# Performance work log

Hardware: AMD Instinct MI355X
Metric: run time of the kernel (lower is better)

Reference implementation:

```python
import jax, jax.numpy as jnp
import numpy as np

EMBED_DIM = 1024
N_HEAD = 16
HEAD_DIM = EMBED_DIM // N_HEAD
B, S = 2, 2048


def setup_inputs() -> dict:
    key = jax.random.key(0)
    ks = jax.random.split(key, 11)
    d = EMBED_DIM
    scale = 1.0 / np.sqrt(d)
    inp = {
        "query_inp": jax.random.normal(ks[0], (B, S, d), dtype=jnp.float32),
        "key_inp": jax.random.normal(ks[1], (B, S, d), dtype=jnp.float32),
        "value_inp": jax.random.normal(ks[2], (B, S, d), dtype=jnp.float32),
        "Wq": jax.random.normal(ks[3], (d, d), dtype=jnp.float32) * scale,
        "bq": jnp.zeros((d,), dtype=jnp.float32),
        "Wk": jax.random.normal(ks[4], (d, d), dtype=jnp.float32) * scale,
        "bk": jnp.zeros((d,), dtype=jnp.float32),
        "Wv": jax.random.normal(ks[5], (d, d), dtype=jnp.float32) * scale,
        "bv": jnp.zeros((d,), dtype=jnp.float32),
        "Wo": jax.random.normal(ks[6], (d, d), dtype=jnp.float32) * scale,
        "bo": jnp.zeros((d,), dtype=jnp.float32),
    }
    return inp


def reference(query_inp, key_inp, value_inp, Wq, bq, Wk, bk, Wv, bv, Wo, bo):
    b, s, _ = query_inp.shape
    # Linear projections (weights stored as [in, out]); split heads -> [b, h, s, hd]
    def proj(x, W, bias):
        y = jnp.einsum("bsd,de->bse", x, W) + bias
        return y.reshape(b, s, N_HEAD, HEAD_DIM).transpose(0, 2, 1, 3)

    q = proj(query_inp, Wq, bq)
    k = proj(key_inp, Wk, bk)
    v = proj(value_inp, Wv, bv)

    scores = jnp.einsum("bhqd,bhkd->bhqk", q, k) / jnp.sqrt(
        jnp.asarray(HEAD_DIM, dtype=q.dtype)
    )
    attn = jax.nn.softmax(scores, axis=-1)
    out = jnp.einsum("bhqk,bhkd->bhqd", attn, v)  # [b, h, s, hd]
    out = out.transpose(0, 2, 1, 3).reshape(b, s, EMBED_DIM)
    return jnp.einsum("bsd,de->bse", out, Wo) + bo
```

## Files before the change

### kernel.cpp

```cpp
#include <hip/hip_runtime.h>


typedef __bf16 bf16;
typedef __bf16 bf16x4 __attribute__((ext_vector_type(4)));
typedef __bf16 bf16x8 __attribute__((ext_vector_type(8)));
typedef float f32x4 __attribute__((ext_vector_type(4)));

#define DEV static __device__ __forceinline__

constexpr int D = 1024;
constexpr int NH = 16;
constexpr int HD = 64;
constexpr int B_ = 2;
constexpr int S_ = 2048;
constexpr size_t MAT = (size_t)D * D;
constexpr size_t XSZ = (size_t)B_ * S_ * D;

DEV void glds16(const bf16* g, bf16* l) {
  __builtin_amdgcn_global_load_lds(
      (__attribute__((address_space(1))) void*)g,
      (__attribute__((address_space(3))) void*)l, 16, 0, 0);
}

DEV int detect_isf(const unsigned short* wq16, int tid) {
  const unsigned short v = wq16[tid & 63];
  const bool hot = ((v >> 7) & 0xFF) >= 0x90;
  return (__ballot(hot) != 0ull) ? 1 : 0;
}

__global__ __launch_bounds__(256) void prep_kernel(
    const void* __restrict__ X0, const void* __restrict__ X1, const void* __restrict__ X2,
    const void* __restrict__ W0, const void* __restrict__ W1,
    const void* __restrict__ W2, const void* __restrict__ W3,
    const void* __restrict__ b0, const void* __restrict__ b1,
    const void* __restrict__ b2, const void* __restrict__ b3,
    const unsigned short* __restrict__ wq16,
    bf16* __restrict__ Xc, bf16* __restrict__ WT4, bf16* __restrict__ bc) {
  __shared__ bf16 t[64][65];
  const int tid = threadIdx.x;
  const int isf = detect_isf(wq16, tid);
  const int blk = blockIdx.x;

  if (blk < 12288) {
    const int mat = blk >> 12;
    const int bx = blk & 4095;
    const void* s = (mat == 0) ? X0 : (mat == 1) ? X1 : X2;
    const size_t vi = (size_t)bx * 256 + tid;
    bf16* dst = Xc + (size_t)mat * XSZ + vi * 4;
    if (isf) {
      const float4 f = ((const float4*)s)[vi];
      bf16x4 o = {(bf16)f.x, (bf16)f.y, (bf16)f.z, (bf16)f.w};
      *(bf16x4*)dst = o;
    } else {
      *(bf16x4*)dst = *(const bf16x4*)((const bf16*)s + vi * 4);
    }
  } else if (blk < 13312) {
    const int idx = blk - 12288;
    const int mat = idx >> 8;
    const int rem = idx & 255;
    const void* W = (mat == 0) ? W0 : (mat == 1) ? W1 : (mat == 2) ? W2 : W3;
    bf16* o = WT4 + (size_t)mat * MAT;
    const int r0 = (rem >> 4) * 64, c0 = (rem & 15) * 64;
#pragma unroll
    for (int e = 0; e < 16; e++) {
      const int ii = tid + e * 256;
      const size_t gi = (size_t)(r0 + (ii >> 6)) * D + c0 + (ii & 63);
      t[ii >> 6][ii & 63] = isf ? (bf16)((const float*)W)[gi] : ((const bf16*)W)[gi];
    }
    __syncthreads();
#pragma unroll
    for (int e = 0; e < 16; e++) {
      const int ii = tid + e * 256;
      const int co = ii >> 6, ro = ii & 63;
      o[(size_t)(c0 + co) * D + r0 + ro] = t[ro][co];
    }
  } else {
    const int mat = blk - 13312;
    const void* s = (mat == 0) ? b0 : (mat == 1) ? b1 : (mat == 2) ? b2 : b3;
    bf16* dst = bc + mat * 1024;
    for (int i = tid; i < 1024; i += 256)
      dst[i] = isf ? (bf16)((const float*)s)[i] : ((const bf16*)s)[i];
  }
}

DEV void gemm_core(const bf16* __restrict__ A, const bf16* __restrict__ WT,
                   int m0, int n0, bf16* As, bf16* Bs, f32x4 acc[4][4]) {
  const int tid = threadIdx.x;
  const int w = tid >> 6, lane = tid & 63;
  const int ln = lane & 15, qd = lane >> 4;
  const int wr = w >> 1, wc = w & 1;
  const int l8r = lane >> 3, l8c = lane & 7;
  const int swz8 = ((l8c ^ l8r) * 8);

#pragma unroll
  for (int i = 0; i < 4; i++)
#pragma unroll
    for (int j = 0; j < 4; j++) acc[i][j] = (f32x4){0.f, 0.f, 0.f, 0.f};

  for (int k0 = 0; k0 < D; k0 += 64) {
    __syncthreads();
#pragma unroll
    for (int t = 0; t < 4; t++) {
      const int c = w * 4 + t;
      glds16(A + (size_t)(m0 + c * 8 + l8r) * D + k0 + swz8, As + c * 512);
      glds16(WT + (size_t)(n0 + c * 8 + l8r) * D + k0 + swz8, Bs + c * 512);
    }
    __syncthreads();
#pragma unroll
    for (int ks = 0; ks < 2; ks++) {
      bf16x8 af[4], bfr[4];
#pragma unroll
      for (int i = 0; i < 4; i++)
        af[i] = *(const bf16x8*)(As + (wr * 64 + i * 16 + ln) * 64 +
                                 (((ks * 4 + qd) ^ (ln & 7)) * 8));
#pragma unroll
      for (int j = 0; j < 4; j++)
        bfr[j] = *(const bf16x8*)(Bs + (wc * 64 + j * 16 + ln) * 64 +
                                  (((ks * 4 + qd) ^ (ln & 7)) * 8));
#pragma unroll
      for (int i = 0; i < 4; i++)
#pragma unroll
        for (int j = 0; j < 4; j++)
          acc[i][j] = __builtin_amdgcn_mfma_f32_16x16x32_bf16(af[i], bfr[j], acc[i][j], 0, 0, 0);
    }
  }
}

__global__ __launch_bounds__(256) void qkv_kernel(
    const bf16* __restrict__ Xc, const bf16* __restrict__ WT4, const bf16* __restrict__ bc,
    bf16* __restrict__ Qb, bf16* __restrict__ Kb, bf16* __restrict__ Vb) {
  __shared__ __align__(16) bf16 SMEM[128 * 128];
  bf16* As = SMEM;
  bf16* Bs = SMEM + 8192;
  const int mt = blockIdx.x;
  const int nb = blockIdx.y;
  const int mat = nb >> 3;
  const int n0 = (nb & 7) * 128;
  const bf16* A = Xc + (size_t)mat * XSZ;
  const bf16* WT = WT4 + (size_t)mat * MAT;
  const bf16* bias = bc + mat * 1024;

  f32x4 acc[4][4];
  gemm_core(A, WT, mt * 128, n0, As, Bs, acc);

  const int tid = threadIdx.x;
  const int w = tid >> 6, lane = tid & 63;
  const int ln = lane & 15, qd = lane >> 4;
  const int wr = w >> 1, wc = w & 1;
  bf16* dst = (mat == 0) ? Qb : (mat == 1) ? Kb : Vb;
  const float scale = (mat == 0) ? 0.180336880f : 1.0f;

  if (mat == 2) {
#pragma unroll
    for (int i = 0; i < 4; i++)
#pragma unroll
      for (int j = 0; j < 4; j++) {
        const int col = n0 + wc * 64 + j * 16 + ln;
        const float bb = (float)bias[col];
        const int h = col >> 6, dd = col & 63;
        const int tok0 = mt * 128 + wr * 64 + i * 16 + qd * 4;
        const int b = tok0 >> 11, s0 = tok0 & (S_ - 1);
        bf16* base = dst + (size_t)(b * NH + h) * S_ * HD;
        bf16x4 pv;
#pragma unroll
        for (int r = 0; r < 4; r++) pv[r] = (bf16)(acc[i][j][r] + bb);
        const size_t off = ((size_t)((dd >> 4) * (S_ >> 5) + (s0 >> 5))) * 512 +
                           ((s0 >> 3) & 3) * 128 + (dd & 15) * 8 + (s0 & 7);
        *(bf16x4*)(base + off) = pv;
      }
  } else {
    __syncthreads();
#pragma unroll
    for (int i = 0; i < 4; i++)
#pragma unroll
      for (int j = 0; j < 4; j++) {
        const int col_local = wc * 64 + j * 16 + ln;
        const float bb = (float)bias[n0 + col_local];
        const int cdd = col_local >> 3, c7 = col_local & 7;
#pragma unroll
        for (int r = 0; r < 4; r++) {
          const int s_local = wr * 64 + i * 16 + qd * 4 + r;
          SMEM[s_local * 128 + ((cdd ^ (s_local & 15)) * 8) + c7] =
              (bf16)((acc[i][j][r] + bb) * scale);
        }
      }
    __syncthreads();
    const int run = tid >> 1;
    const int row16 = run >> 4;
    const int c = run & 15;
    const int hh = (n0 >> 6) + (c >> 3);
    const int b = mt >> 4;
    bf16* gbase = dst + (size_t)(b * NH + hh) * S_ * HD +
                  (size_t)((mt & 15) * 8 + row16) * 1024 + (c & 7) * 128;
    const int sh = (tid & 1) * 8;
#pragma unroll
    for (int e = 0; e < 8; e++) {
      const int srem = sh + e;
      const bf16x8 v =
          *(const bf16x8*)(SMEM + (row16 * 16 + srem) * 128 + ((c ^ srem) & 15) * 8);
      *(bf16x8*)(gbase + srem * 8) = v;
    }
  }
}

__global__ __launch_bounds__(256, 3) void attn_kernel(const bf16* __restrict__ Qb,
                                                      const bf16* __restrict__ Kb,
                                                      const bf16* __restrict__ Vb,
                                                      bf16* __restrict__ Opart,
                                                      float* __restrict__ lbuf) {
  __shared__ __align__(16) bf16 KVs[2][8192];
  __shared__ __align__(16) bf16 P2[64 * 128];

  const int bh = blockIdx.x;
  const int qt = blockIdx.y;
  const int sp = blockIdx.z;
  const int tid = threadIdx.x;
  const int w = tid >> 6, lane = tid & 63;
  const int ln = lane & 15, qd = lane >> 4;

  const size_t base = (size_t)bh * S_ * HD;
  const int q0 = qt * 64;
  const bf16* Kp = Kb + base;
  const bf16* Vp = Vb + base;
  const bf16* Qp = Qb + base;
  bf16* Pw = P2 + (w * 16) * 128;

  bf16x8 qf[2];
#pragma unroll
  for (int t = 0; t < 2; t++)
    qf[t] = *(const bf16x8*)(Qp + (size_t)(qt * 4 + w) * 1024 + (t * 4 + qd) * 128 + ln * 8);

  f32x4 acc_o[4];
#pragma unroll
  for (int j = 0; j < 4; j++) acc_o[j] = (f32x4){0.f, 0.f, 0.f, 0.f};
  float l_i = 0.f;

  const int kbeg = sp * (S_ / 2), kend = kbeg + (S_ / 2);

#define STAGE_KV(buf, k0)                                                              \
  {                                                                                    \
    bf16* Ks_ = &KVs[buf][0];                                                          \
    bf16* Vs_ = &KVs[buf][4096];                                                       \
    _Pragma("unroll") for (int e = 0; e < 2; e++) {                                    \
      const int seg = w * 2 + e;                                                       \
      glds16(Kp + (size_t)((k0) >> 4) * 1024 + seg * 512 + lane * 8, Ks_ + seg * 512); \
    }                                                                                  \
    _Pragma("unroll") for (int s = 0; s < 2; s++) {                                    \
      glds16(Vp + (size_t)(w * (S_ >> 5) + ((k0) >> 5) + s) * 512 + lane * 8,          \
             Vs_ + (w * 2 + s) * 512);                                                 \
    }                                                                                  \
  }

  STAGE_KV(0, kbeg);
  __syncthreads();

  int cur = 0;
  for (int k0 = kbeg; k0 < kend; k0 += 64) {
    if (k0 + 64 < kend) STAGE_KV(cur ^ 1, k0 + 64);

    const bf16* Ks = &KVs[cur][0];
    const bf16* Vs = &KVs[cur][4096];

    f32x4 st[4];
#pragma unroll
    for (int j = 0; j < 4; j++) st[j] = (f32x4){0.f, 0.f, 0.f, 0.f};

    {
      bf16x8 kf[8];
#pragma unroll
      for (int t = 0; t < 2; t++)
#pragma unroll
        for (int j = 0; j < 4; j++)
          kf[t * 4 + j] = *(const bf16x8*)(Ks + j * 1024 + (t * 4 + qd) * 128 + ln * 8);
      __builtin_amdgcn_s_setprio(1);
#pragma unroll
      for (int t = 0; t < 2; t++)
#pragma unroll
        for (int j = 0; j < 4; j++)
          st[j] = __builtin_amdgcn_mfma_f32_16x16x32_bf16(kf[t * 4 + j], qf[t], st[j], 0, 0, 0);
      __builtin_amdgcn_s_setprio(0);
    }

    {
      float rs = 0.f;
#pragma unroll
      for (int j = 0; j < 4; j++)
#pragma unroll
        for (int r = 0; r < 4; r++) {
          const float p = __builtin_amdgcn_exp2f(st[j][r]);
          st[j][r] = p;
          rs += p;
        }
      rs += __shfl_xor(rs, 16);
      rs += __shfl_xor(rs, 32);
      l_i += rs;

      bf16* pr = Pw + ln * 128;
#pragma unroll
      for (int j = 0; j < 4; j++) {
        bf16x4 pv;
#pragma unroll
        for (int r = 0; r < 4; r++) pv[r] = (bf16)st[j][r];
        const int c0 = j * 2 + (qd >> 1);
        *(bf16x4*)(pr + (((c0 + ln) & 15) * 8) + (qd & 1) * 4) = pv;
      }
    }

#pragma unroll
    for (int s = 0; s < 2; s++) {
      bf16x8 vf[4];
#pragma unroll
      for (int jn = 0; jn < 4; jn++)
        vf[jn] = *(const bf16x8*)(Vs + (jn * 2 + s) * 512 + qd * 128 + ln * 8);
      const bf16x8 pf =
          *(const bf16x8*)(Pw + ln * 128 + (((s * 4 + qd + ln) & 15) * 8));
      __builtin_amdgcn_s_setprio(1);
#pragma unroll
      for (int jn = 0; jn < 4; jn++)
        acc_o[jn] = __builtin_amdgcn_mfma_f32_16x16x32_bf16(pf, vf[jn], acc_o[jn], 0, 0, 0);
      __builtin_amdgcn_s_setprio(0);
    }

    __syncthreads();
    cur ^= 1;
  }

  bf16* tw = Pw;
#pragma unroll
  for (int jn = 0; jn < 4; jn++)
#pragma unroll
    for (int r = 0; r < 4; r++)
      tw[(qd * 4 + r) * 72 + jn * 16 + ln] = (bf16)acc_o[jn][r];
  bf16* Og = Opart + (size_t)sp * XSZ + base + (size_t)(q0 + w * 16) * HD;
#pragma unroll
  for (int p = 0; p < 2; p++) {
    const int ql = p * 8 + (lane >> 3);
    const int seg = lane & 7;
    const bf16x8 vv = *(const bf16x8*)(tw + ql * 72 + seg * 8);
    *(bf16x8*)(Og + (size_t)ql * 64 + seg * 8) = vv;
  }
  if (qd == 0)
    lbuf[((size_t)sp * 32 + bh) * S_ + q0 + w * 16 + ln] = l_i;
#undef STAGE_KV
}

__global__ __launch_bounds__(256) void merge_k(const bf16* __restrict__ Opart,
                                               const float* __restrict__ lbuf,
                                               bf16* __restrict__ Ob) {
  const int gid = blockIdx.x * 256 + threadIdx.x;
  const int seg = gid & 7;
  const int row = gid >> 3;
  const int bh = row >> 11, q = row & 2047;
  const float l0 = lbuf[row];
  const float l1 = lbuf[32 * S_ + row];
  const float inv = 1.0f / (l0 + l1);
  const bf16x8 a = *(const bf16x8*)(Opart + (size_t)row * 64 + seg * 8);
  const bf16x8 c = *(const bf16x8*)(Opart + XSZ + (size_t)row * 64 + seg * 8);
  bf16x8 o;
#pragma unroll
  for (int r = 0; r < 8; r++) o[r] = (bf16)(((float)a[r] + (float)c[r]) * inv);
  const int b = bh >> 4, h = bh & 15;
  *(bf16x8*)(Ob + ((size_t)(b * S_ + q)) * D + h * HD + seg * 8) = o;
}

__global__ __launch_bounds__(256) void oproj_kernel(const bf16* __restrict__ Ob,
                                                    const bf16* __restrict__ WoT,
                                                    const bf16* __restrict__ bo,
                                                    const unsigned short* __restrict__ wq16,
                                                    void* __restrict__ outv) {
  __shared__ __align__(16) bf16 As[128 * 64];
  __shared__ __align__(16) bf16 Bs[128 * 64];
  const int isf = detect_isf(wq16, threadIdx.x);
  const int mt = blockIdx.x, nb = blockIdx.y;
  f32x4 acc[4][4];
  gemm_core(Ob, WoT, mt * 128, nb * 128, As, Bs, acc);
  const int tid = threadIdx.x;
  const int w = tid >> 6, lane = tid & 63;
  const int ln = lane & 15, qd = lane >> 4;
  const int wr = w >> 1, wc = w & 1;
#pragma unroll
  for (int i = 0; i < 4; i++)
#pragma unroll
    for (int j = 0; j < 4; j++) {
      const int col = nb * 128 + wc * 64 + j * 16 + ln;
      const float bb = (float)bo[col];
#pragma unroll
      for (int r = 0; r < 4; r++) {
        const int tok = mt * 128 + wr * 64 + i * 16 + qd * 4 + r;
        const float v = acc[i][j][r] + bb;
        const size_t oi = (size_t)tok * D + col;
        if (isf) ((float*)outv)[oi] = v;
        else ((bf16*)outv)[oi] = (bf16)v;
      }
    }
}

extern "C" void kernel_launch(void* const* d_in, const int* in_sizes, int n_in,
                              void* d_out, int out_size, void* d_ws, size_t ws_size,
                              hipStream_t stream) {
  bf16* ws = (bf16*)d_ws;

  bf16* WT4 = ws;
  bf16* Xc  = WT4 + 4 * MAT;
  bf16* bc  = Xc + 3 * XSZ;
  bf16* Qb  = bc + 4096;
  bf16* Kb  = Qb + XSZ;
  bf16* Vb  = Kb + XSZ;
  bf16* Ob  = Vb + XSZ;
  bf16*  Opart = Xc;
  float* lbuf  = (float*)(Xc + 2 * XSZ);

  const unsigned short* wq16 = (const unsigned short*)d_in[3];

  prep_kernel<<<13316, 256, 0, stream>>>(d_in[0], d_in[1], d_in[2],
                                         d_in[3], d_in[5], d_in[7], d_in[9],
                                         d_in[4], d_in[6], d_in[8], d_in[10],
                                         wq16, Xc, WT4, bc);
  qkv_kernel<<<dim3(32, 24), 256, 0, stream>>>(Xc, WT4, bc, Qb, Kb, Vb);
  attn_kernel<<<dim3(32, 32, 2), 256, 0, stream>>>(Qb, Kb, Vb, Opart, lbuf);
  merge_k<<<2048, 256, 0, stream>>>(Opart, lbuf, Ob);
  oproj_kernel<<<dim3(32, 8), 256, 0, stream>>>(Ob, WT4 + 3 * MAT, bc + 3 * 1024, wq16, d_out);
}
```

Measured before the change: 253.4 us.

## Drop split-K attention and merge kernel; normalize output inside attention

Attention blocks now walk the full key length instead of splitting it in two. Each block normalizes its own output by the row sum and writes straight into the head-interleaved Ob layout. This removes the partial-output and row-sum writes, the separate merge kernel launch and its global memory round trip. In exchange the grid halves to 1024 blocks, which lowers parallelism and lengthens each block's serial loop over keys.

```diff
diff --git a/kernel.cpp b/kernel.cpp
--- a/kernel.cpp
+++ b/kernel.cpp
@@ -206,14 +206,12 @@
 __global__ __launch_bounds__(256, 3) void attn_kernel(const bf16* __restrict__ Qb,
                                                       const bf16* __restrict__ Kb,
                                                       const bf16* __restrict__ Vb,
-                                                      bf16* __restrict__ Opart,
-                                                      float* __restrict__ lbuf) {
+                                                      bf16* __restrict__ Ob) {
   __shared__ __align__(16) bf16 KVs[2][8192];
   __shared__ __align__(16) bf16 P2[64 * 128];
 
   const int bh = blockIdx.x;
   const int qt = blockIdx.y;
-  const int sp = blockIdx.z;
   const int tid = threadIdx.x;
   const int w = tid >> 6, lane = tid & 63;
   const int ln = lane & 15, qd = lane >> 4;
@@ -234,8 +232,6 @@
 #pragma unroll
   for (int j = 0; j < 4; j++) acc_o[j] = (f32x4){0.f, 0.f, 0.f, 0.f};
   float l_i = 0.f;
-
-  const int kbeg = sp * (S_ / 2), kend = kbeg + (S_ / 2);
 
 #define STAGE_KV(buf, k0)                                                              \
   {                                                                                    \
@@ -251,12 +247,12 @@
     }                                                                                  \
   }
 
-  STAGE_KV(0, kbeg);
+  STAGE_KV(0, 0);
   __syncthreads();
 
   int cur = 0;
-  for (int k0 = kbeg; k0 < kend; k0 += 64) {
-    if (k0 + 64 < kend) STAGE_KV(cur ^ 1, k0 + 64);
+  for (int k0 = 0; k0 < S_; k0 += 64) {
+    if (k0 + 64 < S_) STAGE_KV(cur ^ 1, k0 + 64);
 
     const bf16* Ks = &KVs[cur][0];
     const bf16* Vs = &KVs[cur][4096];
@@ -325,42 +321,27 @@
     cur ^= 1;
   }
 
+  float inv[4];
+#pragma unroll
+  for (int r = 0; r < 4; r++) inv[r] = 1.0f / __shfl(l_i, qd * 4 + r);
+
   bf16* tw = Pw;
 #pragma unroll
   for (int jn = 0; jn < 4; jn++)
 #pragma unroll
     for (int r = 0; r < 4; r++)
-      tw[(qd * 4 + r) * 72 + jn * 16 + ln] = (bf16)acc_o[jn][r];
-  bf16* Og = Opart + (size_t)sp * XSZ + base + (size_t)(q0 + w * 16) * HD;
+      tw[(qd * 4 + r) * 72 + jn * 16 + ln] = (bf16)(acc_o[jn][r] * inv[r]);
+
+  const int b = bh >> 4, h = bh & 15;
+  bf16* Og = Ob + ((size_t)(b * S_ + q0 + w * 16)) * D + h * HD;
 #pragma unroll
   for (int p = 0; p < 2; p++) {
     const int ql = p * 8 + (lane >> 3);
     const int seg = lane & 7;
     const bf16x8 vv = *(const bf16x8*)(tw + ql * 72 + seg * 8);
-    *(bf16x8*)(Og + (size_t)ql * 64 + seg * 8) = vv;
-  }
-  if (qd == 0)
-    lbuf[((size_t)sp * 32 + bh) * S_ + q0 + w * 16 + ln] = l_i;
+    *(bf16x8*)(Og + (size_t)ql * D + seg * 8) = vv;
+  }
 #undef STAGE_KV
-}
-
-__global__ __launch_bounds__(256) void merge_k(const bf16* __restrict__ Opart,
-                                               const float* __restrict__ lbuf,
-                                               bf16* __restrict__ Ob) {
-  const int gid = blockIdx.x * 256 + threadIdx.x;
-  const int seg = gid & 7;
-  const int row = gid >> 3;
-  const int bh = row >> 11, q = row & 2047;
-  const float l0 = lbuf[row];
-  const float l1 = lbuf[32 * S_ + row];
-  const float inv = 1.0f / (l0 + l1);
-  const bf16x8 a = *(const bf16x8*)(Opart + (size_t)row * 64 + seg * 8);
-  const bf16x8 c = *(const bf16x8*)(Opart + XSZ + (size_t)row * 64 + seg * 8);
-  bf16x8 o;
-#pragma unroll
-  for (int r = 0; r < 8; r++) o[r] = (bf16)(((float)a[r] + (float)c[r]) * inv);
-  const int b = bh >> 4, h = bh & 15;
-  *(bf16x8*)(Ob + ((size_t)(b * S_ + q)) * D + h * HD + seg * 8) = o;
 }
 
 __global__ __launch_bounds__(256) void oproj_kernel(const bf16* __restrict__ Ob,
@@ -407,8 +388,6 @@
   bf16* Kb  = Qb + XSZ;
   bf16* Vb  = Kb + XSZ;
   bf16* Ob  = Vb + XSZ;
-  bf16*  Opart = Xc;
-  float* lbuf  = (float*)(Xc + 2 * XSZ);
 
   const unsigned short* wq16 = (const unsigned short*)d_in[3];
 
@@ -417,7 +396,6 @@
                                          d_in[4], d_in[6], d_in[8], d_in[10],
                                          wq16, Xc, WT4, bc);
   qkv_kernel<<<dim3(32, 24), 256, 0, stream>>>(Xc, WT4, bc, Qb, Kb, Vb);
-  attn_kernel<<<dim3(32, 32, 2), 256, 0, stream>>>(Qb, Kb, Vb, Opart, lbuf);
-  merge_k<<<2048, 256, 0, stream>>>(Opart, lbuf, Ob);
+  attn_kernel<<<dim3(32, 32), 256, 0, stream>>>(Qb, Kb, Vb, Ob);
   oproj_kernel<<<dim3(32, 8), 256, 0, stream>>>(Ob, WT4 + 3 * MAT, bc + 3 * 1024, wq16, d_out);
 }
```

Result: no change. 255.5 us (+0.8%).
